# Kernel optimization log

Hardware: AMD Instinct MI355X
Metric: run time of the kernel (lower is better)

## Reference

```python
import jax, jax.numpy as jnp
import numpy as np

N_NODES = 50000
N_EDGES = 1_600_000
F = 64      # num_edge_features
NH = 3      # n_h hidden blocks
BN_EPS = 1e-5


def setup_inputs() -> dict:
    key = jax.random.key(0)
    ks = jax.random.split(key, 8)
    edge_attr = jax.random.normal(ks[0], (N_EDGES, F), jnp.float32)
    nbr_shift = 0.1 * jax.random.normal(ks[1], (N_EDGES, 3), jnp.float32)
    pos = 10.0 * jax.random.normal(ks[2], (N_NODES, 3), jnp.float32)
    edge_index = jax.random.randint(ks[3], (2, N_EDGES), 0, N_NODES, dtype=jnp.int64)
    Ws = jax.random.normal(ks[4], (NH, F, F), jnp.float32) / np.sqrt(F).astype(np.float32)
    bs = jnp.zeros((NH, F), jnp.float32)
    gammas = jnp.ones((NH, F), jnp.float32)
    betas = jnp.zeros((NH, F), jnp.float32)
    w_out = jax.random.normal(ks[5], (F,), jnp.float32) / np.sqrt(F).astype(np.float32)
    b_out = jnp.zeros((1,), jnp.float32)
    return {"edge_attr": edge_attr, "nbr_shift": nbr_shift, "pos": pos,
            "Ws": Ws, "bs": bs, "gammas": gammas, "betas": betas,
            "w_out": w_out, "b_out": b_out, "edge_index": edge_index}


def _batchnorm(x, gamma, beta):
    # training-mode BatchNorm1d: batch mean / biased variance over edges
    mu = jnp.mean(x, axis=0)
    var = jnp.mean(jnp.square(x - mu), axis=0)
    return gamma * (x - mu) * jax.lax.rsqrt(var + BN_EPS) + beta


def reference(edge_attr, nbr_shift, pos, Ws, bs, gammas, betas, w_out, b_out, edge_index):
    j = edge_index[0]  # source atoms
    i = edge_index[1]  # target atoms
    # gather positions by edge, normalized edge direction  [E,3]
    edge_dir = pos[i] + nbr_shift - pos[j]
    edge_len = jnp.sqrt(jnp.sum(jnp.square(edge_dir), axis=-1, keepdims=True))
    edge_dir = edge_dir / edge_len
    h = edge_attr
    for l in range(NH):
        h = _batchnorm(h @ Ws[l] + bs[l], gammas[l], betas[l])
        h = jax.nn.softplus(h)
    s = (h @ w_out)[:, None] + b_out  # [E,1] scalar per edge
    force_e = s * edge_dir            # [E,3]
    # scatter-add edge forces onto target atoms
    force = jax.ops.segment_sum(force_e, i, num_segments=N_NODES)  # [N,3]
    return force
```

## Files before the change

kernel.cpp:

```cpp
#include <hip/hip_runtime.h>
#include <hip/hip_bf16.h>
#include <math.h>

#define F 64
#define TPB 256
#define MTILE 256
#define BN_EPS 1e-5f
#define LGRID 512

#define NB 16
#define RMAX 3136
#define CAP 114688
#define BPB 16
#define SLABSTRIDE (3 * RMAX)

typedef __attribute__((ext_vector_type(8))) short short8;
typedef __attribute__((ext_vector_type(4))) float f32x4;

__device__ __forceinline__ float sp(float x) {
    return fmaxf(x, 0.f) + __logf(1.f + __expf(-fabsf(x)));
}
__device__ __forceinline__ ushort f2bf(float f) {
    __hip_bfloat16 h = __float2bfloat16(f);
    return *reinterpret_cast<ushort*>(&h);
}
__device__ __forceinline__ float bf2f(ushort u) {
    unsigned v = ((unsigned)u) << 16;
    return __builtin_bit_cast(float, v);
}

template <int HAS_ACT>
__global__ __launch_bounds__(TPB, 2)
void layer_mfma(const void* __restrict__ Xv, uint2* __restrict__ Yg,
                const float* __restrict__ W,
                const float* __restrict__ prev_stats,
                const float* __restrict__ gamma_prev,
                const float* __restrict__ beta_prev,
                float* __restrict__ stats_out, int E)
{
    __shared__ short8 Wt[512];
    __shared__ float aca[F], acb[F];
    __shared__ float sh_s[F], sh_q[F];

    const int t  = threadIdx.x;
    const int w  = t >> 6;
    const int l  = t & 63;
    const int ln = l & 15;
    const int q  = l >> 4;

    #pragma unroll
    for (int uu = 0; uu < 2; ++uu) {
        int u = t + uu * 256;
        int kq = u >> 6, n = u & 63;
        short8 pk;
        #pragma unroll
        for (int j = 0; j < 8; ++j)
            pk[j] = (short)f2bf(W[(kq * 8 + j) * F + n]);
        Wt[u] = pk;
    }
    if (t < F) {
        sh_s[t] = 0.f; sh_q[t] = 0.f;
        if (HAS_ACT) {
            float inv_e = 1.f / (float)E;
            float mu = prev_stats[t] * inv_e;
            float var = prev_stats[F + t] * inv_e - mu * mu;
            float a = gamma_prev[t] * rsqrtf(var + BN_EPS);
            aca[t] = a;
            acb[t] = beta_prev[t] - mu * a;
        }
    }
    __syncthreads();

    short8 afr[4][2];
    #pragma unroll
    for (int ni = 0; ni < 4; ++ni)
        #pragma unroll
        for (int ks = 0; ks < 2; ++ks)
            afr[ni][ks] = Wt[(4 * ks + q) * 64 + ni * 16 + ln];

    float ps[16], pq[16];
    #pragma unroll
    for (int p = 0; p < 16; ++p) { ps[p] = 0.f; pq[p] = 0.f; }

    const int ntiles = E >> 8;

    auto store_acc = [&](f32x4 (&acc)[4][4], int tt) {
        const long e0 = (long)tt * MTILE + w * 64;
        #pragma unroll
        for (int ni = 0; ni < 4; ++ni)
            #pragma unroll
            for (int mi = 0; mi < 4; ++mi) {
                const long e = e0 + mi * 16 + ln;
                f32x4 v = acc[ni][mi];
                uint2 u;
                u.x = (uint)f2bf(v[0]) | ((uint)f2bf(v[1]) << 16);
                u.y = (uint)f2bf(v[2]) | ((uint)f2bf(v[3]) << 16);
                Yg[(size_t)(ni * 4 + q) * E + e] = u;
                #pragma unroll
                for (int r = 0; r < 4; ++r) {
                    float x = v[r];
                    ps[ni * 4 + r] += x;
                    pq[ni * 4 + r] = fmaf(x, x, pq[ni * 4 + r]);
                }
            }
    };

    if constexpr (HAS_ACT) {
        const uint2* X = (const uint2*)Xv;
        uint2 xbA[4][2][2], xbB[4][2][2];

        auto load = [&](uint2 (&xb)[4][2][2], int tt) {
            const long eb = (long)tt * MTILE + w * 64;
            #pragma unroll
            for (int mi = 0; mi < 4; ++mi) {
                const long e = eb + mi * 16 + ln;
                #pragma unroll
                for (int ks = 0; ks < 2; ++ks) {
                    xb[mi][ks][0] = X[(size_t)(8 * ks + 2 * q) * E + e];
                    xb[mi][ks][1] = X[(size_t)(8 * ks + 2 * q + 1) * E + e];
                }
            }
        };

        auto process = [&](uint2 (&xb)[4][2][2], int tt) {
            f32x4 acc[4][4];
            #pragma unroll
            for (int ni = 0; ni < 4; ++ni)
                #pragma unroll
                for (int mi = 0; mi < 4; ++mi)
                    acc[ni][mi] = (f32x4){0.f, 0.f, 0.f, 0.f};

            #pragma unroll
            for (int mi = 0; mi < 4; ++mi) {
                short8 bfr[2];
                #pragma unroll
                for (int ks = 0; ks < 2; ++ks) {
                    uint vs[4] = {xb[mi][ks][0].x, xb[mi][ks][0].y,
                                  xb[mi][ks][1].x, xb[mi][ks][1].y};
                    short8 b;
                    #pragma unroll
                    for (int d = 0; d < 4; ++d) {
                        float x0 = bf2f((ushort)(vs[d] & 0xffffu));
                        float x1 = bf2f((ushort)(vs[d] >> 16));
                        int k0 = 32 * ks + 8 * q + 2 * d;
                        b[2*d]   = (short)f2bf(sp(aca[k0]     * x0 + acb[k0]));
                        b[2*d+1] = (short)f2bf(sp(aca[k0 + 1] * x1 + acb[k0 + 1]));
                    }
                    bfr[ks] = b;
                }
                #pragma unroll
                for (int ks = 0; ks < 2; ++ks)
                    #pragma unroll
                    for (int ni = 0; ni < 4; ++ni)
                        acc[ni][mi] = __builtin_amdgcn_mfma_f32_16x16x32_bf16(
                                          afr[ni][ks], bfr[ks], acc[ni][mi], 0, 0, 0);
            }
            store_acc(acc, tt);
        };

        int tile = blockIdx.x;
        load(xbA, tile);
        while (true) {
            const int tB = tile + LGRID;
            const bool haveB = tB < ntiles;
            if (haveB) load(xbB, tB);
            process(xbA, tile);
            if (!haveB) break;
            tile = tB + LGRID;
            if (tile < ntiles) load(xbA, tile);
            process(xbB, tB);
            if (tile >= ntiles) break;
        }
    } else {
        const float4* X4 = (const float4*)Xv;
        float4 xb[4][2][2];

        auto load = [&](int tt) {
            const long eb = (long)tt * MTILE + w * 64;
            #pragma unroll
            for (int mi = 0; mi < 4; ++mi) {
                const long e = eb + mi * 16 + ln;
                #pragma unroll
                for (int ks = 0; ks < 2; ++ks) {
                    xb[mi][ks][0] = X4[(size_t)e * 16 + 8 * ks + 2 * q];
                    xb[mi][ks][1] = X4[(size_t)e * 16 + 8 * ks + 2 * q + 1];
                }
            }
        };

        load(blockIdx.x);
        #pragma unroll 1
        for (int tile = blockIdx.x; tile < ntiles; tile += LGRID) {
            short8 bfr[4][2];
            #pragma unroll
            for (int mi = 0; mi < 4; ++mi)
                #pragma unroll
                for (int ks = 0; ks < 2; ++ks) {
                    float4 f0 = xb[mi][ks][0], f1 = xb[mi][ks][1];
                    short8 b;
                    b[0] = (short)f2bf(f0.x); b[1] = (short)f2bf(f0.y);
                    b[2] = (short)f2bf(f0.z); b[3] = (short)f2bf(f0.w);
                    b[4] = (short)f2bf(f1.x); b[5] = (short)f2bf(f1.y);
                    b[6] = (short)f2bf(f1.z); b[7] = (short)f2bf(f1.w);
                    bfr[mi][ks] = b;
                }
            if (tile + LGRID < ntiles) load(tile + LGRID);

            f32x4 acc[4][4];
            #pragma unroll
            for (int ni = 0; ni < 4; ++ni)
                #pragma unroll
                for (int mi = 0; mi < 4; ++mi)
                    acc[ni][mi] = (f32x4){0.f, 0.f, 0.f, 0.f};
            #pragma unroll
            for (int mi = 0; mi < 4; ++mi)
                #pragma unroll
                for (int ks = 0; ks < 2; ++ks)
                    #pragma unroll
                    for (int ni = 0; ni < 4; ++ni)
                        acc[ni][mi] = __builtin_amdgcn_mfma_f32_16x16x32_bf16(
                                          afr[ni][ks], bfr[mi][ks], acc[ni][mi], 0, 0, 0);
            store_acc(acc, tile);
        }
    }

    #pragma unroll
    for (int p = 0; p < 16; ++p) {
        #pragma unroll
        for (int m = 1; m < 16; m <<= 1) {
            ps[p] += __shfl_xor(ps[p], m);
            pq[p] += __shfl_xor(pq[p], m);
        }
    }
    if (ln == 0) {
        #pragma unroll
        for (int p = 0; p < 16; ++p) {
            int n = (p >> 2) * 16 + q * 4 + (p & 3);
            atomicAdd(&sh_s[n], ps[p]);
            atomicAdd(&sh_q[n], pq[p]);
        }
    }
    __syncthreads();
    if (t < F) {
        unsafeAtomicAdd(&stats_out[t], sh_s[t]);
        unsafeAtomicAdd(&stats_out[F + t], sh_q[t]);
    }
}

__global__ __launch_bounds__(TPB)
void force_bucket(const uint2* __restrict__ Yg, const float* __restrict__ stats,
                  const float* __restrict__ gamma, const float* __restrict__ beta,
                  const float* __restrict__ w_out, const float* __restrict__ b_out,
                  const float* __restrict__ nbr_shift, const float* __restrict__ pos,
                  const int* __restrict__ edge_index,
                  float4* __restrict__ recs, int* __restrict__ gcnt,
                  float* __restrict__ spill, int E, int R)
{
    __shared__ float ac[2 * F];
    __shared__ float wsh[F];
    __shared__ int lcnt[NB], lbase[NB];
    const int t = threadIdx.x;
    if (t < F) {
        float inv_e = 1.f / (float)E;
        float mu = stats[t] * inv_e;
        float var = stats[F + t] * inv_e - mu * mu;
        float a = gamma[t] * rsqrtf(var + BN_EPS);
        ac[t] = a;
        ac[F + t] = beta[t] - mu * a;
        wsh[t] = w_out[t];
    }
    if (t < NB) lcnt[t] = 0;
    __syncthreads();

    const long e = (long)blockIdx.x * TPB + t;
    const bool valid = e < E;
    float4 rec;
    int b = 0, lrank = 0, in_ = 0;

    if (valid) {
        float s = b_out[0];
        #pragma unroll
        for (int nq = 0; nq < 16; ++nq) {
            uint2 u = Yg[(size_t)nq * E + e];
            int k = 4 * nq;
            float x0 = bf2f((ushort)(u.x & 0xffffu));
            float x1 = bf2f((ushort)(u.x >> 16));
            float x2 = bf2f((ushort)(u.y & 0xffffu));
            float x3 = bf2f((ushort)(u.y >> 16));
            s = fmaf(sp(ac[k]     * x0 + ac[F + k]),     wsh[k],     s);
            s = fmaf(sp(ac[k + 1] * x1 + ac[F + k + 1]), wsh[k + 1], s);
            s = fmaf(sp(ac[k + 2] * x2 + ac[F + k + 2]), wsh[k + 2], s);
            s = fmaf(sp(ac[k + 3] * x3 + ac[F + k + 3]), wsh[k + 3], s);
        }

        const int jn = edge_index[e];
        in_ = edge_index[E + e];
        float dx = pos[3 * in_ + 0] + nbr_shift[3 * e + 0] - pos[3 * jn + 0];
        float dy = pos[3 * in_ + 1] + nbr_shift[3 * e + 1] - pos[3 * jn + 1];
        float dz = pos[3 * in_ + 2] + nbr_shift[3 * e + 2] - pos[3 * jn + 2];
        float inv = rsqrtf(dx * dx + dy * dy + dz * dz);
        float fs = s * inv;
        rec.x = fs * dx; rec.y = fs * dy; rec.z = fs * dz;
        rec.w = __int_as_float(in_);

        b = (int)((unsigned)in_ / (unsigned)R);
        lrank = atomicAdd(&lcnt[b], 1);
    }
    __syncthreads();
    if (t < NB) lbase[t] = atomicAdd(&gcnt[t], lcnt[t]);
    __syncthreads();
    if (valid) {
        int idx = lbase[b] + lrank;
        if (idx < CAP) {
            recs[(size_t)b * CAP + idx] = rec;
        } else {
            unsafeAtomicAdd(&spill[3 * in_ + 0], rec.x);
            unsafeAtomicAdd(&spill[3 * in_ + 1], rec.y);
            unsafeAtomicAdd(&spill[3 * in_ + 2], rec.z);
        }
    }
}

__global__ __launch_bounds__(TPB)
void bucket_accum(const float4* __restrict__ recs, const int* __restrict__ gcnt,
                  float* __restrict__ slabs, int R)
{
    __shared__ float acc[SLABSTRIDE];
    const int bucket = blockIdx.x / BPB;
    const int sub    = blockIdx.x - bucket * BPB;
    const int t = threadIdx.x;
    const int len = 3 * R;

    for (int i = t; i < len; i += TPB) acc[i] = 0.f;
    __syncthreads();

    int cnt = gcnt[bucket];
    if (cnt > CAP) cnt = CAP;
    const int nbase = bucket * R;
    const float4* rb = recs + (size_t)bucket * CAP;

    for (int i = sub * TPB + t; i < cnt; i += BPB * TPB) {
        float4 r = rb[i];
        int loc = 3 * (__float_as_int(r.w) - nbase);
        atomicAdd(&acc[loc + 0], r.x);
        atomicAdd(&acc[loc + 1], r.y);
        atomicAdd(&acc[loc + 2], r.z);
    }
    __syncthreads();

    float* out = slabs + (size_t)blockIdx.x * SLABSTRIDE;
    for (int i = t; i < len; i += TPB) out[i] = acc[i];
}

__global__ __launch_bounds__(TPB)
void reduce_out(const float* __restrict__ slabs, const float* __restrict__ spill,
                float* __restrict__ out, int nodes3, int R)
{
    const int i = blockIdx.x * TPB + threadIdx.x;
    if (i >= nodes3) return;
    const int node = i / 3, c = i - 3 * node;
    const int bucket = node / R, loc = node - bucket * R;
    const size_t off = (size_t)(bucket * BPB) * SLABSTRIDE + 3 * loc + c;
    float s = spill[i];
    #pragma unroll
    for (int r = 0; r < BPB; ++r)
        s += slabs[off + (size_t)r * SLABSTRIDE];
    out[i] = s;
}

extern "C" void kernel_launch(void* const* d_in, const int* in_sizes, int n_in,
                              void* d_out, int out_size, void* d_ws, size_t ws_size,
                              hipStream_t stream)
{
    const int E = in_sizes[0] / F;
    const float* edge_attr = (const float*)d_in[0];
    const float* nbr_shift = (const float*)d_in[1];
    const float* pos       = (const float*)d_in[2];
    const float* Ws        = (const float*)d_in[3];
    const float* gammas    = (const float*)d_in[5];
    const float* betas     = (const float*)d_in[6];
    const float* w_out     = (const float*)d_in[7];
    const float* b_out     = (const float*)d_in[8];
    const int*   edge_index= (const int*)d_in[9];

    const int nodes3 = out_size;
    const int nodes  = nodes3 / 3;
    const int R = (nodes + NB - 1) / NB;

    char* p = (char*)d_ws;
    const size_t SZY = (size_t)E * F * 2;
    uint2* Y1 = (uint2*)p;                 p += SZY;
    uint2* Y2 = (uint2*)p;                 p += SZY;
    float* stats = (float*)p;              p += 4096;
    float4* recs = (float4*)p;             p += (size_t)NB * CAP * 16;
    int*   gcnt  = (int*)p;                p += 256;
    float* slabs = (float*)p;              p += (size_t)NB * BPB * SLABSTRIDE * 4;
    float* spill = (float*)p;              p += (size_t)nodes3 * 4;

    hipMemsetAsync(stats, 0, 6 * F * sizeof(float), stream);
    hipMemsetAsync(gcnt, 0, 256, stream);
    hipMemsetAsync(spill, 0, (size_t)nodes3 * sizeof(float), stream);

    layer_mfma<0><<<LGRID, TPB, 0, stream>>>(edge_attr, Y1, Ws,
                                             nullptr, nullptr, nullptr, stats, E);
    layer_mfma<1><<<LGRID, TPB, 0, stream>>>(Y1, Y2, Ws + F * F,
                                             stats, gammas, betas, stats + 2 * F, E);
    layer_mfma<1><<<LGRID, TPB, 0, stream>>>(Y2, Y1, Ws + 2 * F * F,
                                             stats + 2 * F, gammas + F, betas + F,
                                             stats + 4 * F, E);
    force_bucket<<<(E + TPB - 1) / TPB, TPB, 0, stream>>>(
        Y1, stats + 4 * F, gammas + 2 * F, betas + 2 * F, w_out, b_out,
        nbr_shift, pos, edge_index, recs, gcnt, spill, E, R);
    bucket_accum<<<NB * BPB, TPB, 0, stream>>>(recs, gcnt, slabs, R);
    reduce_out<<<(nodes3 + TPB - 1) / TPB, TPB, 0, stream>>>(
        slabs, spill, (float*)d_out, nodes3, R);
}
```

Measured before the change: 924.6 us.

## Replace global bucket counters with per-block local sort and prefix offsets

Measured after the change: 899.6 us. 2.7% less time.

```diff
diff --git a/kernel.cpp b/kernel.cpp
--- a/kernel.cpp
+++ b/kernel.cpp
@@ -10,7 +10,6 @@
 
 #define NB 16
 #define RMAX 3136
-#define CAP 114688
 #define BPB 16
 #define SLABSTRIDE (3 * RMAX)
 
@@ -253,12 +252,13 @@
                   const float* __restrict__ w_out, const float* __restrict__ b_out,
                   const float* __restrict__ nbr_shift, const float* __restrict__ pos,
                   const int* __restrict__ edge_index,
-                  float4* __restrict__ recs, int* __restrict__ gcnt,
-                  float* __restrict__ spill, int E, int R)
+                  float4* __restrict__ recs, uint* __restrict__ pref,
+                  int E, int R)
 {
     __shared__ float ac[2 * F];
     __shared__ float wsh[F];
     __shared__ int lcnt[NB], lbase[NB];
+    __shared__ float4 srt[TPB];
     const int t = threadIdx.x;
     if (t < F) {
         float inv_e = 1.f / (float)E;
@@ -273,11 +273,10 @@
     __syncthreads();
 
     const long e = (long)blockIdx.x * TPB + t;
-    const bool valid = e < E;
-    float4 rec;
-    int b = 0, lrank = 0, in_ = 0;
-
-    if (valid) {
+    float4 rec = {0.f, 0.f, 0.f, __int_as_float(0)};
+    int b = 0;
+
+    if (e < E) {
         float s = b_out[0];
         #pragma unroll
         for (int nq = 0; nq < 16; ++nq) {
@@ -293,8 +292,8 @@
             s = fmaf(sp(ac[k + 3] * x3 + ac[F + k + 3]), wsh[k + 3], s);
         }
 
-        const int jn = edge_index[e];
-        in_ = edge_index[E + e];
+        const int jn  = edge_index[e];
+        const int in_ = edge_index[E + e];
         float dx = pos[3 * in_ + 0] + nbr_shift[3 * e + 0] - pos[3 * jn + 0];
         float dy = pos[3 * in_ + 1] + nbr_shift[3 * e + 1] - pos[3 * jn + 1];
         float dz = pos[3 * in_ + 2] + nbr_shift[3 * e + 2] - pos[3 * jn + 2];
@@ -302,28 +301,25 @@
         float fs = s * inv;
         rec.x = fs * dx; rec.y = fs * dy; rec.z = fs * dz;
         rec.w = __int_as_float(in_);
-
         b = (int)((unsigned)in_ / (unsigned)R);
-        lrank = atomicAdd(&lcnt[b], 1);
-    }
-    __syncthreads();
-    if (t < NB) lbase[t] = atomicAdd(&gcnt[t], lcnt[t]);
-    __syncthreads();
-    if (valid) {
-        int idx = lbase[b] + lrank;
-        if (idx < CAP) {
-            recs[(size_t)b * CAP + idx] = rec;
-        } else {
-            unsafeAtomicAdd(&spill[3 * in_ + 0], rec.x);
-            unsafeAtomicAdd(&spill[3 * in_ + 1], rec.y);
-            unsafeAtomicAdd(&spill[3 * in_ + 2], rec.z);
-        }
-    }
+    }
+    int lrank = atomicAdd(&lcnt[b], 1);
+    __syncthreads();
+    if (t < NB) {
+        int sacc = 0;
+        for (int j = 0; j < t; ++j) sacc += lcnt[j];
+        lbase[t] = sacc;
+    }
+    __syncthreads();
+    srt[lbase[b] + lrank] = rec;
+    __syncthreads();
+    recs[(size_t)blockIdx.x * TPB + t] = srt[t];
+    if (t < NB) pref[blockIdx.x * NB + t] = (uint)lbase[t];
 }
 
 __global__ __launch_bounds__(TPB)
-void bucket_accum(const float4* __restrict__ recs, const int* __restrict__ gcnt,
-                  float* __restrict__ slabs, int R)
+void bucket_accum(const float4* __restrict__ recs, const uint* __restrict__ pref,
+                  float* __restrict__ slabs, int R, int nsrc)
 {
     __shared__ float acc[SLABSTRIDE];
     const int bucket = blockIdx.x / BPB;
@@ -334,17 +330,23 @@
     for (int i = t; i < len; i += TPB) acc[i] = 0.f;
     __syncthreads();
 
-    int cnt = gcnt[bucket];
-    if (cnt > CAP) cnt = CAP;
+    const int wv = t >> 6;
+    const int l  = t & 63;
+    const int sg = l >> 4;
+    const int r  = l & 15;
     const int nbase = bucket * R;
-    const float4* rb = recs + (size_t)bucket * CAP;
-
-    for (int i = sub * TPB + t; i < cnt; i += BPB * TPB) {
-        float4 r = rb[i];
-        int loc = 3 * (__float_as_int(r.w) - nbase);
-        atomicAdd(&acc[loc + 0], r.x);
-        atomicAdd(&acc[loc + 1], r.y);
-        atomicAdd(&acc[loc + 2], r.z);
+
+    for (int sb = (sub * 4 + wv) * 4 + sg; sb < nsrc; sb += BPB * 16) {
+        uint st = pref[sb * NB + bucket];
+        uint en = (bucket < NB - 1) ? pref[sb * NB + bucket + 1] : (uint)TPB;
+        const float4* rg = recs + (size_t)sb * TPB;
+        for (uint i = st + r; i < en; i += 16) {
+            float4 rec = rg[i];
+            int loc = 3 * (__float_as_int(rec.w) - nbase);
+            atomicAdd(&acc[loc + 0], rec.x);
+            atomicAdd(&acc[loc + 1], rec.y);
+            atomicAdd(&acc[loc + 2], rec.z);
+        }
     }
     __syncthreads();
 
@@ -353,15 +355,15 @@
 }
 
 __global__ __launch_bounds__(TPB)
-void reduce_out(const float* __restrict__ slabs, const float* __restrict__ spill,
-                float* __restrict__ out, int nodes3, int R)
+void reduce_out(const float* __restrict__ slabs, float* __restrict__ out,
+                int nodes3, int R)
 {
     const int i = blockIdx.x * TPB + threadIdx.x;
     if (i >= nodes3) return;
     const int node = i / 3, c = i - 3 * node;
     const int bucket = node / R, loc = node - bucket * R;
     const size_t off = (size_t)(bucket * BPB) * SLABSTRIDE + 3 * loc + c;
-    float s = spill[i];
+    float s = 0.f;
     #pragma unroll
     for (int r = 0; r < BPB; ++r)
         s += slabs[off + (size_t)r * SLABSTRIDE];
@@ -386,20 +388,18 @@
     const int nodes3 = out_size;
     const int nodes  = nodes3 / 3;
     const int R = (nodes + NB - 1) / NB;
+    const int nsrc = (E + TPB - 1) / TPB;
 
     char* p = (char*)d_ws;
     const size_t SZY = (size_t)E * F * 2;
     uint2* Y1 = (uint2*)p;                 p += SZY;
     uint2* Y2 = (uint2*)p;                 p += SZY;
     float* stats = (float*)p;              p += 4096;
-    float4* recs = (float4*)p;             p += (size_t)NB * CAP * 16;
-    int*   gcnt  = (int*)p;                p += 256;
+    float4* recs = (float4*)p;             p += (size_t)nsrc * TPB * 16;
+    uint*  pref  = (uint*)p;               p += (size_t)nsrc * NB * 4;
     float* slabs = (float*)p;              p += (size_t)NB * BPB * SLABSTRIDE * 4;
-    float* spill = (float*)p;              p += (size_t)nodes3 * 4;
 
     hipMemsetAsync(stats, 0, 6 * F * sizeof(float), stream);
-    hipMemsetAsync(gcnt, 0, 256, stream);
-    hipMemsetAsync(spill, 0, (size_t)nodes3 * sizeof(float), stream);
 
     layer_mfma<0><<<LGRID, TPB, 0, stream>>>(edge_attr, Y1, Ws,
                                              nullptr, nullptr, nullptr, stats, E);
@@ -408,10 +408,10 @@
     layer_mfma<1><<<LGRID, TPB, 0, stream>>>(Y2, Y1, Ws + 2 * F * F,
                                              stats + 2 * F, gammas + F, betas + F,
                                              stats + 4 * F, E);
-    force_bucket<<<(E + TPB - 1) / TPB, TPB, 0, stream>>>(
+    force_bucket<<<nsrc, TPB, 0, stream>>>(
         Y1, stats + 4 * F, gammas + 2 * F, betas + 2 * F, w_out, b_out,
-        nbr_shift, pos, edge_index, recs, gcnt, spill, E, R);
-    bucket_accum<<<NB * BPB, TPB, 0, stream>>>(recs, gcnt, slabs, R);
+        nbr_shift, pos, edge_index, recs, pref, E, R);
+    bucket_accum<<<NB * BPB, TPB, 0, stream>>>(recs, pref, slabs, R, nsrc);
     reduce_out<<<(nodes3 + TPB - 1) / TPB, TPB, 0, stream>>>(
-        slabs, spill, (float*)d_out, nodes3, R);
-}
+        slabs, (float*)d_out, nodes3, R);
+}
```
